# Kernel optimization log

Hardware: AMD Instinct MI355X
Metric: run time of the kernel (lower is better)

The kernel has to match this reference:

```python
import jax, jax.numpy as jnp
import numpy as np

N_MESH = 40962  # icosahedral level-6 mesh nodes (x[..., -40962:])


def _lin_coords(out_size, in_size, scale):
    # torch F.interpolate bilinear, align_corners=False source coords
    i = jnp.arange(out_size, dtype=jnp.float32)
    src = jnp.maximum((i + 0.5) / scale - 0.5, 0.0)
    i0 = jnp.clip(jnp.floor(src).astype(jnp.int32), 0, in_size - 1)
    i1 = jnp.minimum(i0 + 1, in_size - 1)
    w = src - i0.astype(jnp.float32)
    return i0, i1, w


def _bilinear4(x):
    # x: (B,C,H,W) -> (B,C,4H,4W), separable bilinear, align_corners=False
    B, C, H, W = x.shape
    i0, i1, wh = _lin_coords(4 * H, H, 4.0)
    x = x[:, :, i0, :] * (1.0 - wh)[None, None, :, None] + x[:, :, i1, :] * wh[None, None, :, None]
    j0, j1, ww = _lin_coords(4 * W, W, 4.0)
    x = x[:, :, :, j0] * (1.0 - ww) + x[:, :, :, j1] * ww
    return x


def _grid2mesh(x, lat, lon):
    # x: (B,C,H,W); drop last lat row, upsample x4, append broadcast pole row
    B, C, H, W = x.shape
    pole = x[:, :, -1, 0][:, :, None, None] * jnp.ones((B, C, 1, 4 * W), x.dtype)
    xi = _bilinear4(x[:, :, :-1, :])            # (B,C,4(H-1),4W)
    xi = jnp.concatenate([xi, pole], axis=2)    # (B,C,4(H-1)+1,4W)
    return xi[:, :, lat - 1, lon - 1]           # (B,C,M) gather at mesh coords


def _gcn(h, W, b, src, dst, norm, n):
    # GCNConv: sym-normalized scatter-add aggregation of linearly transformed feats
    h = h @ W                                    # (B,N,Hd)
    msg = lambda hb: jax.ops.segment_sum(hb[src] * norm[:, None], dst, num_segments=n)
    return jax.vmap(msg)(h) + b


def reference(x, edge_index, Lat, Lon, W1, b1, W2, b2, Wl, bl, Wl1, bl1):
    B, C, H, Wd = x.shape
    mesh = _grid2mesh(x, Lat, Lon)                               # (B,C,M)
    feats = jnp.concatenate([x.reshape(B, C, H * Wd), mesh], -1)  # (B,C,N)
    h = feats.transpose(0, 2, 1)                                 # (B,N,C)
    n = h.shape[1]

    # gcn_norm with self loops (edge_weight = 1)
    loops = jnp.arange(n, dtype=edge_index.dtype)
    src = jnp.concatenate([edge_index[0], loops])
    dst = jnp.concatenate([edge_index[1], loops])
    deg = jax.ops.segment_sum(jnp.ones(src.shape, h.dtype), dst, num_segments=n)
    dinv = jnp.where(deg > 0, deg ** -0.5, 0.0)
    norm = dinv[src] * dinv[dst]

    h = _gcn(h, W1, b1, src, dst, norm, n)
    h = jax.nn.gelu(h, approximate=False)
    h = _gcn(h, W2, b2, src, dst, norm, n)
    h = h[:, -N_MESH:, :]                                        # keep mesh nodes
    out = jax.nn.gelu((h @ Wl + bl) @ Wl1 + bl1, approximate=False)
    return out.transpose(0, 2, 1)                                # (B,out_ch,M)


def setup_inputs() -> dict:
    key = jax.random.key(0)
    ks = jax.random.split(key, 16)
    B, C, H, W = 1, 69, 181, 360
    HID, OUT = 256, 256
    N = H * W + N_MESH  # 106122
    E = 500000
    x = jax.random.normal(ks[0], (B, C, H, W), jnp.float32)
    edge_index = jax.random.randint(ks[1], (2, E), 0, N, dtype=jnp.int64)
    Lat = jax.random.randint(ks[2], (N_MESH,), 1, 4 * (H - 1) + 2, dtype=jnp.int64)
    Lon = jax.random.randint(ks[3], (N_MESH,), 1, 4 * W + 1, dtype=jnp.int64)
    s = 0.05
    return {
        "x": x, "edge_index": edge_index, "Lat": Lat, "Lon": Lon,
        "W1": jax.random.normal(ks[4], (C, HID), jnp.float32) * s,
        "b1": jnp.zeros((HID,), jnp.float32),
        "W2": jax.random.normal(ks[5], (HID, HID), jnp.float32) * s,
        "b2": jnp.zeros((HID,), jnp.float32),
        "Wl": jax.random.normal(ks[6], (HID, 256), jnp.float32) * s,
        "bl": jnp.zeros((256,), jnp.float32),
        "Wl1": jax.random.normal(ks[7], (256, OUT), jnp.float32) * s,
        "bl1": jnp.zeros((OUT,), jnp.float32),
    }
```

## Files before the change

kernel.cpp:

```cpp
#include <hip/hip_runtime.h>

#define NGRID 65160
#define NMESH 40962
#define NTOT  (NGRID + NMESH)
#define CIN   69
#define KPAD1 96
#define HID   256
#define HH    181
#define WWID  360
#define SCAN_BS 1024
#define NBLK_SCAN ((NTOT + SCAN_BS - 1) / SCAN_BS)

#define NT1TILES ((NTOT + 63) / 64)
#define NT1PAD   (NT1TILES * 64)
#define NT2TILES ((NMESH + 63) / 64)
#define NT2PAD   (NT2TILES * 64)

#define W1OFF  0
#define WCOFF  (96 * 256)
#define WALLK  (96 + 256)

typedef float f32x4 __attribute__((ext_vector_type(4)));
typedef _Float16 f16;
typedef _Float16 f16x2 __attribute__((ext_vector_type(2)));
typedef _Float16 f16x4 __attribute__((ext_vector_type(4)));
typedef _Float16 f16x8 __attribute__((ext_vector_type(8)));

__device__ __forceinline__ float gelu_exact(float v) {
    return 0.5f * v * (1.0f + erff(v * 0.7071067811865476f));
}
__device__ __forceinline__ float gelu_fast(float v) {
    float u = v * fmaf(v * v, 0.07135481283f, 1.5957691216f);
    return v * __builtin_amdgcn_rcpf(1.0f + __expf(-u));
}

__global__ __launch_bounds__(256) void transpose_x(const float* __restrict__ x,
                                                   f16* __restrict__ h0g) {
    __shared__ float tile[96][65];
    int s0 = blockIdx.x * 64;
    int t = threadIdx.x;
#pragma unroll
    for (int i = 0; i < 24; ++i) {
        int idx = t + i * 256;
        int c = idx >> 6, s = idx & 63;
        int gs = s0 + s;
        float v = 0.f;
        if (c < CIN && gs < NGRID) v = x[(size_t)c * NGRID + gs];
        tile[c][s] = v;
    }
    __syncthreads();
#pragma unroll
    for (int i = 0; i < 12; ++i) {
        int idx = t + i * 256;
        int r = idx / 48, u = idx % 48;
        int gr = s0 + r;
        if (gr < NGRID) {
            f16x2 p;
            p.x = (f16)tile[u * 2 + 0][r];
            p.y = (f16)tile[u * 2 + 1][r];
            ((f16x2*)h0g)[(size_t)gr * 48 + u] = p;
        }
    }
}

__global__ __launch_bounds__(256) void mesh_interp(const f16* __restrict__ h0g,
                                                   const int* __restrict__ Lat,
                                                   const int* __restrict__ Lon,
                                                   f16* __restrict__ h0m) {
    int t = blockIdx.x * 256 + threadIdx.x;
    if (t >= NMESH * 48) return;
    int j = t / 48, u = t % 48;
    int la = Lat[j] - 1;
    int lo = Lon[j] - 1;
    const f16x2* g = (const f16x2*)h0g;
    f16x2 o;
    if (la == 720) {
        o = g[(size_t)(180 * WWID) * 48 + u];
    } else {
        float sh = fmaxf((la + 0.5f) * 0.25f - 0.5f, 0.0f);
        int i0 = min((int)sh, HH - 2);
        int i1 = min(i0 + 1, HH - 2);
        float wh = sh - (float)i0;
        float sw = fmaxf((lo + 0.5f) * 0.25f - 0.5f, 0.0f);
        int j0 = min((int)sw, WWID - 1);
        int j1 = min(j0 + 1, WWID - 1);
        float ww = sw - (float)j0;
        f16x2 v00 = g[(size_t)(i0 * WWID + j0) * 48 + u];
        f16x2 v10 = g[(size_t)(i1 * WWID + j0) * 48 + u];
        f16x2 v01 = g[(size_t)(i0 * WWID + j1) * 48 + u];
        f16x2 v11 = g[(size_t)(i1 * WWID + j1) * 48 + u];
        float ax = (float)v00.x + ((float)v10.x - (float)v00.x) * wh;
        float ay = (float)v00.y + ((float)v10.y - (float)v00.y) * wh;
        float bx = (float)v01.x + ((float)v11.x - (float)v01.x) * wh;
        float by = (float)v01.y + ((float)v11.y - (float)v01.y) * wh;
        o.x = (f16)(ax + (bx - ax) * ww);
        o.y = (f16)(ay + (by - ay) * ww);
    }
    ((f16x2*)h0m)[(size_t)j * 48 + u] = o;
}

__global__ void deg_init(float* __restrict__ deg, int* __restrict__ cnt) {
    int i = blockIdx.x * 256 + threadIdx.x;
    if (i < NTOT) { deg[i] = 1.0f; cnt[i] = 0; }
}
__global__ void deg_scatter(const int* __restrict__ ei, float* __restrict__ deg, int E) {
    int e = blockIdx.x * 256 + threadIdx.x;
    if (e < E) atomicAdd(&deg[ei[E + e]], 1.0f);
}

__global__ __launch_bounds__(SCAN_BS) void scan1(const float* __restrict__ deg,
                                                 float* __restrict__ dinv,
                                                 int* __restrict__ off, int* __restrict__ bsum) {
    __shared__ int s[SCAN_BS];
    int t = threadIdx.x;
    int i = blockIdx.x * SCAN_BS + t;
    int v = (i < NTOT) ? ((int)deg[i] - 1) : 0;
    if (i < NTOT) dinv[i] = 1.0f / sqrtf((float)(v + 1));
    s[t] = v; __syncthreads();
    for (int d = 1; d < SCAN_BS; d <<= 1) {
        int x = (t >= d) ? s[t - d] : 0;
        __syncthreads();
        s[t] += x;
        __syncthreads();
    }
    if (i < NTOT) off[i] = s[t] - v;
    if (t == SCAN_BS - 1) bsum[blockIdx.x] = s[t];
}
__global__ void scan2(int* __restrict__ bsum) {
    __shared__ int s[128];
    int t = threadIdx.x;
    int v = (t < NBLK_SCAN) ? bsum[t] : 0;
    s[t] = v; __syncthreads();
    for (int d = 1; d < 128; d <<= 1) {
        int x = (t >= d) ? s[t - d] : 0;
        __syncthreads();
        s[t] += x;
        __syncthreads();
    }
    if (t < NBLK_SCAN) bsum[t] = s[t] - v;
}
__global__ __launch_bounds__(SCAN_BS) void scan3(int* __restrict__ off, const int* __restrict__ bsum) {
    int i = blockIdx.x * SCAN_BS + threadIdx.x;
    if (i < NTOT) off[i] += bsum[blockIdx.x];
}

__global__ void csr_fill(const int* __restrict__ ei, const float* __restrict__ dinv,
                         const int* __restrict__ off, int* __restrict__ cnt,
                         int2* __restrict__ epk, int E) {
    int e = blockIdx.x * 256 + threadIdx.x;
    if (e >= E) return;
    int s = ei[e], d = ei[E + e];
    int pos = off[d] + atomicAdd(&cnt[d], 1);
    epk[pos] = make_int2(s, __float_as_int(dinv[s] * dinv[d]));
}

__global__ __launch_bounds__(256) void wgemm(const float* __restrict__ A,
                                             const float* __restrict__ B,
                                             float* __restrict__ C) {
    __shared__ float As[16][68];
    __shared__ float Bs[16][64];
    int r0 = blockIdx.y * 64, c0 = blockIdx.x * 64;
    int t = threadIdx.x;
    int tr = t >> 4, tc = t & 15;
    float acc[4][4] = {};
    for (int kk = 0; kk < 256; kk += 16) {
#pragma unroll
        for (int i = 0; i < 4; ++i) {
            int idx = t + i * 256;
            int r = idx >> 4, k = idx & 15;
            As[k][r] = A[(size_t)(r0 + r) * 256 + kk + k];
        }
#pragma unroll
        for (int i = 0; i < 4; ++i) {
            int idx = t + i * 256;
            int k = idx >> 6, c = idx & 63;
            Bs[k][c] = B[(size_t)(kk + k) * 256 + c0 + c];
        }
        __syncthreads();
#pragma unroll
        for (int k = 0; k < 16; ++k) {
            float a[4], b[4];
#pragma unroll
            for (int i = 0; i < 4; ++i) a[i] = As[k][tr * 4 + i];
#pragma unroll
            for (int j = 0; j < 4; ++j) b[j] = Bs[k][tc * 4 + j];
#pragma unroll
            for (int i = 0; i < 4; ++i)
#pragma unroll
                for (int j = 0; j < 4; ++j) acc[i][j] = fmaf(a[i], b[j], acc[i][j]);
        }
        __syncthreads();
    }
#pragma unroll
    for (int i = 0; i < 4; ++i)
#pragma unroll
        for (int j = 0; j < 4; ++j)
            C[(size_t)(r0 + tr * 4 + i) * 256 + c0 + tc * 4 + j] = acc[i][j];
}

__global__ __launch_bounds__(256) void bias_k(const float* __restrict__ b2,
                                              const float* __restrict__ M1,
                                              const float* __restrict__ bl,
                                              const float* __restrict__ Wl1,
                                              const float* __restrict__ bl1,
                                              float* __restrict__ bc) {
    int c = threadIdx.x;
    float acc = bl1[c];
    for (int j = 0; j < 256; ++j) {
        acc = fmaf(b2[j], M1[(size_t)j * 256 + c], acc);
        acc = fmaf(bl[j], Wl1[(size_t)j * 256 + c], acc);
    }
    bc[c] = acc;
}

__global__ void pack_f16(const float* __restrict__ W1, const float* __restrict__ Wc,
                         f16* __restrict__ wp) {
    int t = blockIdx.x * 256 + threadIdx.x;
    if (t >= WALLK * HID) return;
    int kg = t >> 8, c = t & 255;
    float v;
    size_t idx;
    if (kg < 96) {
        v = (kg < CIN) ? W1[(size_t)kg * HID + c] : 0.f;
        idx = W1OFF + ((((size_t)(kg >> 3)) * HID + c) << 3) + (kg & 7);
    } else {
        int ks = kg - 96;
        int kl = ((ks & 15) << 4) | (ks >> 4);
        v = Wc[(size_t)kl * HID + c];
        idx = WCOFF + ((((size_t)(ks >> 3)) * HID + c) << 3) + (ks & 7);
    }
    wp[idx] = (f16)v;
}

__global__ __launch_bounds__(256) void agg1(const f16* __restrict__ h0,
                                            const float* __restrict__ deg,
                                            const float* __restrict__ dinv,
                                            const int* __restrict__ off,
                                            const int2* __restrict__ epk,
                                            f16* __restrict__ P0) {
    int wv = (blockIdx.x * 256 + threadIdx.x) >> 6;
    if (wv >= NT1PAD) return;
    int lane = threadIdx.x & 63;
    if (lane >= 48) return;
    int r = wv & 63, tile = wv >> 6;
    char* dst = (char*)P0 + (size_t)tile * 12288 + ((r * 192 + lane * 4) ^ ((r & 7) << 4));
    if (wv >= NTOT) { *(unsigned*)dst = 0u; return; }
    int d = wv;
    const f16x2* g = (const f16x2*)h0;
    float dv = dinv[d];
    float w2 = dv * dv;
    f16x2 v = g[(size_t)d * 48 + lane];
    float ax = w2 * (float)v.x;
    float ay = w2 * (float)v.y;
    const int2* ep = epk + off[d];
    int n = (int)deg[d] - 1;
    int p = 0;
    for (; p + 4 <= n; p += 4) {
        int2 e0 = ep[p], e1 = ep[p + 1], e2 = ep[p + 2], e3 = ep[p + 3];
        f16x2 u0 = g[(size_t)e0.x * 48 + lane];
        f16x2 u1 = g[(size_t)e1.x * 48 + lane];
        f16x2 u2 = g[(size_t)e2.x * 48 + lane];
        f16x2 u3 = g[(size_t)e3.x * 48 + lane];
        float w0 = __int_as_float(e0.y), w1 = __int_as_float(e1.y);
        float w2b = __int_as_float(e2.y), w3 = __int_as_float(e3.y);
        ax = fmaf(w0, (float)u0.x, ax); ay = fmaf(w0, (float)u0.y, ay);
        ax = fmaf(w1, (float)u1.x, ax); ay = fmaf(w1, (float)u1.y, ay);
        ax = fmaf(w2b, (float)u2.x, ax); ay = fmaf(w2b, (float)u2.y, ay);
        ax = fmaf(w3, (float)u3.x, ax); ay = fmaf(w3, (float)u3.y, ay);
    }
    for (; p < n; ++p) {
        int2 e = ep[p];
        f16x2 u = g[(size_t)e.x * 48 + lane];
        float w = __int_as_float(e.y);
        ax = fmaf(w, (float)u.x, ax);
        ay = fmaf(w, (float)u.y, ay);
    }
    f16x2 o; o.x = (f16)ax; o.y = (f16)ay;
    *(f16x2*)dst = o;
}

__global__ __launch_bounds__(256) void agg2(const f16* __restrict__ A,
                                            const float* __restrict__ deg,
                                            const float* __restrict__ dinv,
                                            const int* __restrict__ off,
                                            const int2* __restrict__ epk,
                                            f16* __restrict__ P2) {
    int wv = (blockIdx.x * 256 + threadIdx.x) >> 6;
    if (wv >= NT2PAD) return;
    int lane = threadIdx.x & 63;
    int r = wv & 63, tile = wv >> 6;
    char* dst = (char*)P2 + (size_t)tile * 32768 + ((r * 512 + lane * 8) ^ ((r & 7) << 4));
    if (wv >= NMESH) { *(unsigned long long*)dst = 0ull; return; }
    int d = NGRID + wv;
    const f16x4* g = (const f16x4*)A;
    float dv = dinv[d];
    float w2 = dv * dv;
    f16x4 v = g[(size_t)d * 64 + lane];
    float4 acc;
    acc.x = w2 * (float)v.x; acc.y = w2 * (float)v.y;
    acc.z = w2 * (float)v.z; acc.w = w2 * (float)v.w;
    const int2* ep = epk + off[d];
    int n = (int)deg[d] - 1;
    int p = 0;
    for (; p + 4 <= n; p += 4) {
        int2 e0 = ep[p], e1 = ep[p + 1], e2 = ep[p + 2], e3 = ep[p + 3];
        f16x4 u0 = g[(size_t)e0.x * 64 + lane];
        f16x4 u1 = g[(size_t)e1.x * 64 + lane];
        f16x4 u2 = g[(size_t)e2.x * 64 + lane];
        f16x4 u3 = g[(size_t)e3.x * 64 + lane];
        float w0 = __int_as_float(e0.y), w1 = __int_as_float(e1.y);
        float w2b = __int_as_float(e2.y), w3 = __int_as_float(e3.y);
        acc.x = fmaf(w0, (float)u0.x, acc.x); acc.y = fmaf(w0, (float)u0.y, acc.y);
        acc.z = fmaf(w0, (float)u0.z, acc.z); acc.w = fmaf(w0, (float)u0.w, acc.w);
        acc.x = fmaf(w1, (float)u1.x, acc.x); acc.y = fmaf(w1, (float)u1.y, acc.y);
        acc.z = fmaf(w1, (float)u1.z, acc.z); acc.w = fmaf(w1, (float)u1.w, acc.w);
        acc.x = fmaf(w2b, (float)u2.x, acc.x); acc.y = fmaf(w2b, (float)u2.y, acc.y);
        acc.z = fmaf(w2b, (float)u2.z, acc.z); acc.w = fmaf(w2b, (float)u2.w, acc.w);
        acc.x = fmaf(w3, (float)u3.x, acc.x); acc.y = fmaf(w3, (float)u3.y, acc.y);
        acc.z = fmaf(w3, (float)u3.z, acc.z); acc.w = fmaf(w3, (float)u3.w, acc.w);
    }
    for (; p < n; ++p) {
        int2 e = ep[p];
        f16x4 u = g[(size_t)e.x * 64 + lane];
        float w = __int_as_float(e.y);
        acc.x = fmaf(w, (float)u.x, acc.x); acc.y = fmaf(w, (float)u.y, acc.y);
        acc.z = fmaf(w, (float)u.z, acc.z); acc.w = fmaf(w, (float)u.w, acc.w);
    }
    f16x4 o;
    o.x = (f16)acc.x; o.y = (f16)acc.y; o.z = (f16)acc.z; o.w = (f16)acc.w;
    *(f16x4*)dst = o;
}

__global__ __launch_bounds__(256) void gemm1_f16(const f16* __restrict__ P0,
                                                 const f16* __restrict__ wp,
                                                 const float* __restrict__ bias,
                                                 f16* __restrict__ Af) {
    const int wid = (blockIdx.x * 256 + threadIdx.x) >> 6;
    const int lane = threadIdx.x & 63;
    const int l15 = lane & 15, l4 = lane >> 4;
    const int tile = wid >> 3;
    const int rb = (wid >> 1) & 3;
    const int ch = wid & 1;
    if (tile >= NT1TILES) return;

    f16x8 a[3];
    {
        const char* base = (const char*)P0 + (size_t)tile * 12288;
        int r = rb * 16 + l15;
#pragma unroll
        for (int ks = 0; ks < 3; ++ks) {
            int byte = r * 192 + (ks * 32 + l4 * 8) * 2;
            a[ks] = *(const f16x8*)(base + (byte ^ ((r & 7) << 4)));
        }
    }

    f32x4 acc[8];
#pragma unroll
    for (int j = 0; j < 8; ++j) acc[j] = (f32x4)0.f;
#pragma unroll
    for (int j = 0; j < 8; ++j) {
        int c = (ch * 8 + j) * 16 + l15;
#pragma unroll
        for (int ks = 0; ks < 3; ++ks) {
            size_t o = ((((size_t)ks << 2) + l4) * HID + c) << 3;
            f16x8 w = *(const f16x8*)(wp + W1OFF + o);
            acc[j] = __builtin_amdgcn_mfma_f32_16x16x32_f16(a[ks], w, acc[j], 0, 0, 0);
        }
    }

    float bv[8];
#pragma unroll
    for (int j = 0; j < 8; ++j) bv[j] = bias[(ch * 8 + j) * 16 + l15];

    const int gr0 = tile * 64 + rb * 16 + l4 * 4;
#pragma unroll
    for (int reg = 0; reg < 4; ++reg) {
        int gr = gr0 + reg;
        if (gr < NTOT) {
            f16x8 o;
#pragma unroll
            for (int j = 0; j < 8; ++j)
                o[j] = (f16)gelu_fast(acc[j][reg] + bv[j]);
            *(f16x8*)(Af + (size_t)gr * HID + l15 * 16 + ch * 8) = o;
        }
    }
}

__global__ __launch_bounds__(256) void final_k(const f16* __restrict__ P2,
                                               const f16* __restrict__ wp,
                                               const float* __restrict__ bc,
                                               float* __restrict__ out) {
    __shared__ __align__(16) f16 Ps[64 * 256];
    const int tile = blockIdx.x;
    const int row0 = tile * 64;
    const int t = threadIdx.x;
    const int lane = t & 63;
    const int wave = t >> 6;
    const int l15 = lane & 15, l4 = lane >> 4;
    const int cw = wave * 64;
    const char* src = (const char*)P2 + (size_t)tile * 32768;
#pragma unroll
    for (int i = 0; i < 8; ++i) {
        int o = t * 16 + i * 4096;
        *(uint4*)((char*)Ps + o) = *(const uint4*)(src + o);
    }
    __syncthreads();
    f32x4 acc[4][4] = {};
#pragma unroll
    for (int ks = 0; ks < 256; ks += 32) {
        f16x8 w[4], p[4];
#pragma unroll
        for (int mb = 0; mb < 4; ++mb) {
            int c = cw + mb * 16 + l15;
            size_t off = ((((size_t)ks >> 3) + l4) * HID + c) << 3;
            w[mb] = *(const f16x8*)(wp + WCOFF + off);
        }
#pragma unroll
        for (int jb = 0; jb < 4; ++jb) {
            int r = jb * 16 + l15;
            int byte = r * 512 + (ks + l4 * 8) * 2;
            int swz = byte ^ ((r & 7) << 4);
            p[jb] = *(f16x8*)((char*)Ps + swz);
        }
#pragma unroll
        for (int mb = 0; mb < 4; ++mb)
#pragma unroll
            for (int jb = 0; jb < 4; ++jb)
                acc[mb][jb] = __builtin_amdgcn_mfma_f32_16x16x32_f16(w[mb], p[jb], acc[mb][jb], 0, 0, 0);
    }
    const bool full = (row0 + 64 <= NMESH);
#pragma unroll
    for (int mb = 0; mb < 4; ++mb) {
#pragma unroll
        for (int r = 0; r < 4; ++r) {
            int c = cw + mb * 16 + l4 * 4 + r;
            float bv = bc[c];
            float* orow = out + (size_t)c * NMESH + row0;
#pragma unroll
            for (int jb = 0; jb < 4; ++jb) {
                int j = jb * 16 + l15;
                float v = gelu_fast(acc[mb][jb][r] + bv);
                if (full || row0 + j < NMESH) orow[j] = v;
            }
        }
    }
}

extern "C" void kernel_launch(void* const* d_in, const int* in_sizes, int n_in,
                              void* d_out, int out_size, void* d_ws, size_t ws_size,
                              hipStream_t stream) {
    const float* x   = (const float*)d_in[0];
    const int*   ei  = (const int*)d_in[1];
    const int*   Lat = (const int*)d_in[2];
    const int*   Lon = (const int*)d_in[3];
    const float* W1  = (const float*)d_in[4];
    const float* b1  = (const float*)d_in[5];
    const float* W2  = (const float*)d_in[6];
    const float* b2  = (const float*)d_in[7];
    const float* Wl  = (const float*)d_in[8];
    const float* bl  = (const float*)d_in[9];
    const float* Wl1 = (const float*)d_in[10];
    const float* bl1 = (const float*)d_in[11];
    float* out = (float*)d_out;
    const int E = in_sizes[1] / 2;

    f16*   h0  = (f16*)d_out;
    int2*  epk = (int2*)((char*)d_out + (size_t)NTOT * KPAD1 * 2);

    f16*   P0   = (f16*)d_ws;
    f16*   Af   = P0 + (size_t)NT1TILES * 6144;
    f16*   P2   = Af + (size_t)NTOT * HID;
    float* deg  = (float*)(P2 + (size_t)NT2TILES * 16384);
    float* dinv = deg + NTOT;
    int*   off  = (int*)(dinv + NTOT);
    int*   cnt  = off + NTOT;
    int*   bsum = cnt + NTOT;
    float* M1   = (float*)(bsum + 128);
    float* WcF  = M1 + HID * HID;
    float* bc   = WcF + HID * HID;
    f16*   wp   = (f16*)(bc + HID);

    transpose_x<<<(NGRID + 63) / 64, 256, 0, stream>>>(x, h0);
    mesh_interp<<<(NMESH * 48 + 255) / 256, 256, 0, stream>>>(h0, Lat, Lon,
                                                              h0 + (size_t)NGRID * KPAD1);

    deg_init<<<(NTOT + 255) / 256, 256, 0, stream>>>(deg, cnt);
    deg_scatter<<<(E + 255) / 256, 256, 0, stream>>>(ei, deg, E);
    scan1<<<NBLK_SCAN, SCAN_BS, 0, stream>>>(deg, dinv, off, bsum);
    scan2<<<1, 128, 0, stream>>>(bsum);
    scan3<<<NBLK_SCAN, SCAN_BS, 0, stream>>>(off, bsum);
    csr_fill<<<(E + 255) / 256, 256, 0, stream>>>(ei, dinv, off, cnt, epk, E);

    dim3 gW(4, 4);
    wgemm<<<gW, 256, 0, stream>>>(Wl, Wl1, M1);
    wgemm<<<gW, 256, 0, stream>>>(W2, M1, WcF);
    bias_k<<<1, 256, 0, stream>>>(b2, M1, bl, Wl1, bl1, bc);
    pack_f16<<<(WALLK * HID + 255) / 256, 256, 0, stream>>>(W1, WcF, wp);

    agg1<<<(int)(((long long)NT1PAD * 64 + 255) / 256), 256, 0, stream>>>(
        h0, deg, dinv, off, epk, P0);
    gemm1_f16<<<(NT1TILES * 8 * 64 + 255) / 256, 256, 0, stream>>>(P0, wp, b1, Af);

    agg2<<<(int)(((long long)NT2PAD * 64 + 255) / 256), 256, 0, stream>>>(
        Af, deg, dinv, off, epk, P2);

    final_k<<<NT2TILES, 256, 0, stream>>>(P2, wp, bc, out);
}
```

Measured before the change: 242.1 us.

## Pad CSR rows to multiples of four and merge small setup kernels

Measured after the change: 242.6 us. Within noise of the previous version (+0.2%).

```diff
diff --git a/kernel.cpp b/kernel.cpp
--- a/kernel.cpp
+++ b/kernel.cpp
@@ -3,6 +3,7 @@
 #define NGRID 65160
 #define NMESH 40962
 #define NTOT  (NGRID + NMESH)
+#define ZROW  NTOT
 #define CIN   69
 #define KPAD1 96
 #define HID   256
@@ -16,6 +17,9 @@
 #define NT2TILES ((NMESH + 63) / 64)
 #define NT2PAD   (NT2TILES * 64)
 
+#define TXBLKS  ((NGRID + 63) / 64)
+#define DEGBLKS ((NTOT + 255) / 256)
+
 #define W1OFF  0
 #define WCOFF  (96 * 256)
 #define WALLK  (96 + 256)
@@ -26,16 +30,30 @@
 typedef _Float16 f16x4 __attribute__((ext_vector_type(4)));
 typedef _Float16 f16x8 __attribute__((ext_vector_type(8)));
 
-__device__ __forceinline__ float gelu_exact(float v) {
-    return 0.5f * v * (1.0f + erff(v * 0.7071067811865476f));
-}
 __device__ __forceinline__ float gelu_fast(float v) {
     float u = v * fmaf(v * v, 0.07135481283f, 1.5957691216f);
     return v * __builtin_amdgcn_rcpf(1.0f + __expf(-u));
 }
 
+__global__ void prep_pad(int2* __restrict__ epk, unsigned* __restrict__ h0z,
+                         unsigned* __restrict__ Afz, int padmax) {
+    int i = blockIdx.x * 256 + threadIdx.x;
+    if (i < padmax) epk[i] = make_int2(ZROW, 0);
+    if (blockIdx.x == 0) {
+        if (threadIdx.x < 48)  h0z[threadIdx.x] = 0u;
+        if (threadIdx.x < 128) Afz[threadIdx.x] = 0u;
+    }
+}
+
 __global__ __launch_bounds__(256) void transpose_x(const float* __restrict__ x,
-                                                   f16* __restrict__ h0g) {
+                                                   f16* __restrict__ h0g,
+                                                   float* __restrict__ deg,
+                                                   int* __restrict__ cnt) {
+    if (blockIdx.x >= TXBLKS) {
+        int i = (blockIdx.x - TXBLKS) * 256 + threadIdx.x;
+        if (i < NTOT) { deg[i] = 1.0f; cnt[i] = 0; }
+        return;
+    }
     __shared__ float tile[96][65];
     int s0 = blockIdx.x * 64;
     int t = threadIdx.x;
@@ -99,10 +117,6 @@
     ((f16x2*)h0m)[(size_t)j * 48 + u] = o;
 }
 
-__global__ void deg_init(float* __restrict__ deg, int* __restrict__ cnt) {
-    int i = blockIdx.x * 256 + threadIdx.x;
-    if (i < NTOT) { deg[i] = 1.0f; cnt[i] = 0; }
-}
 __global__ void deg_scatter(const int* __restrict__ ei, float* __restrict__ deg, int E) {
     int e = blockIdx.x * 256 + threadIdx.x;
     if (e < E) atomicAdd(&deg[ei[E + e]], 1.0f);
@@ -115,33 +129,33 @@
     int t = threadIdx.x;
     int i = blockIdx.x * SCAN_BS + t;
     int v = (i < NTOT) ? ((int)deg[i] - 1) : 0;
+    int vp = (v + 3) & ~3;
     if (i < NTOT) dinv[i] = 1.0f / sqrtf((float)(v + 1));
-    s[t] = v; __syncthreads();
+    s[t] = vp; __syncthreads();
     for (int d = 1; d < SCAN_BS; d <<= 1) {
         int x = (t >= d) ? s[t - d] : 0;
         __syncthreads();
         s[t] += x;
         __syncthreads();
     }
-    if (i < NTOT) off[i] = s[t] - v;
+    if (i < NTOT) off[i] = s[t] - vp;
     if (t == SCAN_BS - 1) bsum[blockIdx.x] = s[t];
 }
-__global__ void scan2(int* __restrict__ bsum) {
+__global__ __launch_bounds__(SCAN_BS) void scan3(int* __restrict__ off, const int* __restrict__ bsum) {
     __shared__ int s[128];
     int t = threadIdx.x;
-    int v = (t < NBLK_SCAN) ? bsum[t] : 0;
-    s[t] = v; __syncthreads();
+    if (t < 128) s[t] = (t < NBLK_SCAN) ? bsum[t] : 0;
+    __syncthreads();
     for (int d = 1; d < 128; d <<= 1) {
-        int x = (t >= d) ? s[t - d] : 0;
+        int x = 0;
+        if (t < 128 && t >= d) x = s[t - d];
         __syncthreads();
-        s[t] += x;
+        if (t < 128) s[t] += x;
         __syncthreads();
     }
-    if (t < NBLK_SCAN) bsum[t] = s[t] - v;
-}
-__global__ __launch_bounds__(SCAN_BS) void scan3(int* __restrict__ off, const int* __restrict__ bsum) {
-    int i = blockIdx.x * SCAN_BS + threadIdx.x;
-    if (i < NTOT) off[i] += bsum[blockIdx.x];
+    int base = (blockIdx.x == 0) ? 0 : s[blockIdx.x - 1];
+    int i = blockIdx.x * SCAN_BS + t;
+    if (i < NTOT) off[i] += base;
 }
 
 __global__ void csr_fill(const int* __restrict__ ei, const float* __restrict__ dinv,
@@ -253,9 +267,8 @@
     float ax = w2 * (float)v.x;
     float ay = w2 * (float)v.y;
     const int2* ep = epk + off[d];
-    int n = (int)deg[d] - 1;
-    int p = 0;
-    for (; p + 4 <= n; p += 4) {
+    int np = (((int)deg[d] - 1) + 3) & ~3;
+    for (int p = 0; p < np; p += 4) {
         int2 e0 = ep[p], e1 = ep[p + 1], e2 = ep[p + 2], e3 = ep[p + 3];
         f16x2 u0 = g[(size_t)e0.x * 48 + lane];
         f16x2 u1 = g[(size_t)e1.x * 48 + lane];
@@ -267,13 +280,6 @@
         ax = fmaf(w1, (float)u1.x, ax); ay = fmaf(w1, (float)u1.y, ay);
         ax = fmaf(w2b, (float)u2.x, ax); ay = fmaf(w2b, (float)u2.y, ay);
         ax = fmaf(w3, (float)u3.x, ax); ay = fmaf(w3, (float)u3.y, ay);
-    }
-    for (; p < n; ++p) {
-        int2 e = ep[p];
-        f16x2 u = g[(size_t)e.x * 48 + lane];
-        float w = __int_as_float(e.y);
-        ax = fmaf(w, (float)u.x, ax);
-        ay = fmaf(w, (float)u.y, ay);
     }
     f16x2 o; o.x = (f16)ax; o.y = (f16)ay;
     *(f16x2*)dst = o;
@@ -300,9 +306,8 @@
     acc.x = w2 * (float)v.x; acc.y = w2 * (float)v.y;
     acc.z = w2 * (float)v.z; acc.w = w2 * (float)v.w;
     const int2* ep = epk + off[d];
-    int n = (int)deg[d] - 1;
-    int p = 0;
-    for (; p + 4 <= n; p += 4) {
+    int np = (((int)deg[d] - 1) + 3) & ~3;
+    for (int p = 0; p < np; p += 4) {
         int2 e0 = ep[p], e1 = ep[p + 1], e2 = ep[p + 2], e3 = ep[p + 3];
         f16x4 u0 = g[(size_t)e0.x * 64 + lane];
         f16x4 u1 = g[(size_t)e1.x * 64 + lane];
@@ -318,13 +323,6 @@
         acc.z = fmaf(w2b, (float)u2.z, acc.z); acc.w = fmaf(w2b, (float)u2.w, acc.w);
         acc.x = fmaf(w3, (float)u3.x, acc.x); acc.y = fmaf(w3, (float)u3.y, acc.y);
         acc.z = fmaf(w3, (float)u3.z, acc.z); acc.w = fmaf(w3, (float)u3.w, acc.w);
-    }
-    for (; p < n; ++p) {
-        int2 e = ep[p];
-        f16x4 u = g[(size_t)e.x * 64 + lane];
-        float w = __int_as_float(e.y);
-        acc.x = fmaf(w, (float)u.x, acc.x); acc.y = fmaf(w, (float)u.y, acc.y);
-        acc.z = fmaf(w, (float)u.z, acc.z); acc.w = fmaf(w, (float)u.w, acc.w);
     }
     f16x4 o;
     o.x = (f16)acc.x; o.y = (f16)acc.y; o.z = (f16)acc.z; o.w = (f16)acc.w;
@@ -463,13 +461,14 @@
     const float* bl1 = (const float*)d_in[11];
     float* out = (float*)d_out;
     const int E = in_sizes[1] / 2;
+    const int padmax = E + 3 * NTOT + 4;
 
     f16*   h0  = (f16*)d_out;
-    int2*  epk = (int2*)((char*)d_out + (size_t)NTOT * KPAD1 * 2);
+    int2*  epk = (int2*)((char*)d_out + (size_t)(NTOT + 1) * KPAD1 * 2);
 
     f16*   P0   = (f16*)d_ws;
     f16*   Af   = P0 + (size_t)NT1TILES * 6144;
-    f16*   P2   = Af + (size_t)NTOT * HID;
+    f16*   P2   = Af + (size_t)(NTOT + 1) * HID;
     float* deg  = (float*)(P2 + (size_t)NT2TILES * 16384);
     float* dinv = deg + NTOT;
     int*   off  = (int*)(dinv + NTOT);
@@ -480,14 +479,16 @@
     float* bc   = WcF + HID * HID;
     f16*   wp   = (f16*)(bc + HID);
 
-    transpose_x<<<(NGRID + 63) / 64, 256, 0, stream>>>(x, h0);
+    prep_pad<<<(padmax + 255) / 256, 256, 0, stream>>>(
+        epk, (unsigned*)(h0 + (size_t)NTOT * KPAD1),
+        (unsigned*)(Af + (size_t)NTOT * HID), padmax);
+
+    transpose_x<<<TXBLKS + DEGBLKS, 256, 0, stream>>>(x, h0, deg, cnt);
     mesh_interp<<<(NMESH * 48 + 255) / 256, 256, 0, stream>>>(h0, Lat, Lon,
                                                               h0 + (size_t)NGRID * KPAD1);
 
-    deg_init<<<(NTOT + 255) / 256, 256, 0, stream>>>(deg, cnt);
     deg_scatter<<<(E + 255) / 256, 256, 0, stream>>>(ei, deg, E);
     scan1<<<NBLK_SCAN, SCAN_BS, 0, stream>>>(deg, dinv, off, bsum);
-    scan2<<<1, 128, 0, stream>>>(bsum);
     scan3<<<NBLK_SCAN, SCAN_BS, 0, stream>>>(off, bsum);
     csr_fill<<<(E + 255) / 256, 256, 0, stream>>>(ei, dinv, off, cnt, epk, E);
 
```
